# Kernel optimization log

Hardware: AMD Instinct MI355X
Metric: run time of the kernel (lower is better)

Reference implementation:

```python
import jax, jax.numpy as jnp
import numpy as np

D_MODEL = 1024
NUM_HEADS = 16
D_K = D_MODEL // NUM_HEADS
THETA = 10000.0


def _rope(x, pos):
    # x: [B, H, S, D_K], pos: [S]
    angles = 1.0 / (THETA ** (jnp.arange(0, D_K, 2, dtype=jnp.float32) / D_K))  # [D_K/2]
    ang = pos.astype(jnp.float32)[:, None] * angles  # [S, D_K/2]
    cos = jnp.repeat(jnp.cos(ang), 2, axis=-1)  # [S, D_K]
    sin = jnp.repeat(jnp.sin(ang), 2, axis=-1)
    x2 = x.reshape(*x.shape[:-1], D_K // 2, 2)
    xr = jnp.stack([-x2[..., 1], x2[..., 0]], axis=-1).reshape(x.shape)
    return x * cos + xr * sin


def setup_inputs() -> dict:
    key = jax.random.key(0)
    ks = jax.random.split(key, 5)
    B, S = 2, 2048
    sd = np.sqrt(2.0 / (D_MODEL + D_MODEL))
    return {
        "x": jax.random.normal(ks[0], (B, S, D_MODEL), dtype=jnp.float32),
        "token_positions": jnp.arange(S, dtype=jnp.int32),
        "Wq": jax.random.normal(ks[1], (D_MODEL, D_MODEL), dtype=jnp.float32) * sd,
        "Wk": jax.random.normal(ks[2], (D_MODEL, D_MODEL), dtype=jnp.float32) * sd,
        "Wv": jax.random.normal(ks[3], (D_MODEL, D_MODEL), dtype=jnp.float32) * sd,
        "Wo": jax.random.normal(ks[4], (D_MODEL, D_MODEL), dtype=jnp.float32) * sd,
    }


def reference(x, token_positions, Wq, Wk, Wv, Wo):
    B, S, _ = x.shape

    def proj_heads(W):
        y = jnp.einsum('bsd,ed->bse', x, W)  # weight stored [d_out, d_in]
        return y.reshape(B, S, NUM_HEADS, D_K).transpose(0, 2, 1, 3)  # [B,H,S,Dk]

    q = _rope(proj_heads(Wq), token_positions)
    k = _rope(proj_heads(Wk), token_positions)
    v = proj_heads(Wv)

    scores = jnp.einsum('bhqd,bhkd->bhqk', q, k) / np.sqrt(D_K)  # [B,H,S,S]
    causal = jnp.tril(jnp.ones((S, S), dtype=bool))
    scores = jnp.where(causal, scores, -jnp.inf)
    attn = jax.nn.softmax(scores, axis=-1)
    out = jnp.einsum('bhqk,bhkd->bhqd', attn, v)  # [B,H,S,Dk]
    out = out.transpose(0, 2, 1, 3).reshape(B, S, D_MODEL)
    return jnp.einsum('bsd,ed->bse', out, Wo)
```

## Files before the change

kernel.cpp:

```cpp
#include <hip/hip_runtime.h>
#include <hip/hip_bf16.h>
#include <cstdint>
#include <cmath>

#define SEQ 2048
#define NH 16
#define DM 1024
#define BATCH 2

typedef short bf16x8 __attribute__((ext_vector_type(8)));
typedef float f32x4 __attribute__((ext_vector_type(4)));
typedef const void __attribute__((address_space(1)))* gas_t;
typedef void __attribute__((address_space(3)))* las_t;

#if __has_builtin(__builtin_amdgcn_exp2f)
#define EXP2(x) __builtin_amdgcn_exp2f(x)
#else
#define EXP2(x) __expf((x) * 0.6931471805599453f)
#endif

#define QSCALE 0.18033688011112042f

static __device__ __forceinline__ unsigned short f2bf(float f) {
    union { __hip_bfloat16 h; unsigned short u; } cv;
    cv.h = __float2bfloat16(f);
    return cv.u;
}
static __device__ __forceinline__ float bf2f(unsigned short u) {
    union { unsigned short u; __hip_bfloat16 h; } cv;
    cv.u = u;
    return __bfloat162float(cv.h);
}

static __device__ __forceinline__ void gload_lds16(const void* g, void* l) {
    __builtin_amdgcn_global_load_lds(
        reinterpret_cast<gas_t>(reinterpret_cast<uintptr_t>(g)),
        reinterpret_cast<las_t>(reinterpret_cast<uintptr_t>(l)),
        16, 0, 0);
}

__global__ __launch_bounds__(256) void cvt_all(
    const float* __restrict__ x,  const float* __restrict__ wq,
    const float* __restrict__ wk, const float* __restrict__ wv,
    const float* __restrict__ wo,
    unsigned short* __restrict__ xb, unsigned short* __restrict__ wqkv,
    unsigned short* __restrict__ wob) {
    int blk = blockIdx.x;
    const float* src; unsigned short* dst; int base;
    if (blk < 4096)      { src = x;  dst = xb;              base = blk; }
    else if (blk < 5120) { src = wq; dst = wqkv;            base = blk - 4096; }
    else if (blk < 6144) { src = wk; dst = wqkv + 1048576;  base = blk - 5120; }
    else if (blk < 7168) { src = wv; dst = wqkv + 2097152;  base = blk - 6144; }
    else                 { src = wo; dst = wob;             base = blk - 7168; }
    int i = base * 256 + threadIdx.x;
    float4 v = reinterpret_cast<const float4*>(src)[i];
    ushort4 o;
    o.x = f2bf(v.x); o.y = f2bf(v.y); o.z = f2bf(v.z); o.w = f2bf(v.w);
    reinterpret_cast<ushort4*>(dst)[i] = o;
}

template<int OUT_BF16>
__global__ __launch_bounds__(256) void gemm_bt(
    const unsigned short* __restrict__ A,
    const unsigned short* __restrict__ B,
    void* __restrict__ C, int M, int N, int K) {
    __shared__ unsigned short As[128 * 32];
    __shared__ unsigned short Bs[128 * 32];
    const int tid = threadIdx.x;
    const int lane = tid & 63, wid = tid >> 6;
    const int wr = wid >> 1, wc = wid & 1;
    const int ln15 = lane & 15, kq = lane >> 4;
    const int bm = blockIdx.y, bn = blockIdx.x;

    f32x4 acc[4][4] = {};
    const int nk = K >> 5;
    for (int kt = 0; kt < nk; ++kt) {
        #pragma unroll
        for (int i = 0; i < 2; ++i) {
            int c = i * 256 + tid;
            int row = c >> 2, k8 = (c & 3) << 3;
            size_t gofsA = (size_t)(bm * 128 + row) * K + kt * 32 + k8;
            size_t gofsB = (size_t)(bn * 128 + row) * K + kt * 32 + k8;
            unsigned ldsoff = (unsigned)(i * 256 + wid * 64) * 16;
            gload_lds16(A + gofsA, (char*)As + ldsoff);
            gload_lds16(B + gofsB, (char*)Bs + ldsoff);
        }
        __syncthreads();
        bf16x8 af[4], bf[4];
        #pragma unroll
        for (int m = 0; m < 4; ++m)
            af[m] = *reinterpret_cast<const bf16x8*>(&As[(wr * 64 + m * 16 + ln15) * 32 + kq * 8]);
        #pragma unroll
        for (int n = 0; n < 4; ++n)
            bf[n] = *reinterpret_cast<const bf16x8*>(&Bs[(wc * 64 + n * 16 + ln15) * 32 + kq * 8]);
        #pragma unroll
        for (int m = 0; m < 4; ++m)
            #pragma unroll
            for (int n = 0; n < 4; ++n)
                acc[m][n] = __builtin_amdgcn_mfma_f32_16x16x32_bf16(af[m], bf[n], acc[m][n], 0, 0, 0);
        __syncthreads();
    }
    #pragma unroll
    for (int m = 0; m < 4; ++m) {
        #pragma unroll
        for (int n = 0; n < 4; ++n) {
            int col = bn * 128 + wc * 64 + n * 16 + ln15;
            #pragma unroll
            for (int j = 0; j < 4; ++j) {
                int row = bm * 128 + wr * 64 + m * 16 + kq * 4 + j;
                if constexpr (OUT_BF16 != 0)
                    ((unsigned short*)C)[(size_t)row * N + col] = f2bf(acc[m][n][j]);
                else
                    ((float*)C)[(size_t)row * N + col] = acc[m][n][j];
            }
        }
    }
}

__global__ __launch_bounds__(256) void rope_table(const int* __restrict__ pos,
                                                  float2* __restrict__ tab) {
    int idx = blockIdx.x * 256 + threadIdx.x;
    int s = idx >> 5, i = idx & 31;
    float fpos = (float)pos[s];
    float freq = exp2f(-(float)i * (13.287712379549449f / 32.0f));
    float ang = fpos * freq, sn, cs;
    sincosf(ang, &sn, &cs);
    tab[idx] = make_float2(cs, sn);
}

__global__ __launch_bounds__(256) void rope_kernel(
    const unsigned short* __restrict__ qkv, const float2* __restrict__ tab,
    unsigned short* __restrict__ Qh, unsigned short* __restrict__ Kh) {
    int bs = blockIdx.x;
    int b = bs >> 11, s = bs & (SEQ - 1);
    int t = threadIdx.x;
    #pragma unroll
    for (int p = t; p < 512; p += 256) {
        int h = p >> 5, i = p & 31;
        float2 cs = tab[(s << 5) + i];
        size_t src = (size_t)bs * 3072 + h * 64 + 2 * i;
        size_t dst = ((size_t)(b * NH + h) * SEQ + s) * 64 + 2 * i;
        ushort2 qv = *reinterpret_cast<const ushort2*>(qkv + src);
        float q0 = bf2f(qv.x), q1 = bf2f(qv.y);
        ushort2 qo;
        qo.x = f2bf((q0 * cs.x - q1 * cs.y) * QSCALE);
        qo.y = f2bf((q1 * cs.x + q0 * cs.y) * QSCALE);
        *reinterpret_cast<ushort2*>(Qh + dst) = qo;
        ushort2 kv = *reinterpret_cast<const ushort2*>(qkv + src + 1024);
        float k0 = bf2f(kv.x), k1 = bf2f(kv.y);
        ushort2 ko;
        ko.x = f2bf(k0 * cs.x - k1 * cs.y);
        ko.y = f2bf(k1 * cs.x + k0 * cs.y);
        *reinterpret_cast<ushort2*>(Kh + dst) = ko;
    }
}

__global__ __launch_bounds__(256) void vtrans_kernel(
    const unsigned short* __restrict__ qkv, unsigned short* __restrict__ Vo) {
    __shared__ unsigned short tile[64][65];
    int blk = blockIdx.x;
    int st = blk & 31, bh = blk >> 5;
    int sb = st * 64;
    int t = threadIdx.x;
    int b = bh >> 4, h = bh & 15;
    #pragma unroll
    for (int u = t; u < 1024; u += 256) {
        int sl = u >> 4, d4 = (u & 15) << 2;
        ushort4 v = *reinterpret_cast<const ushort4*>(
            qkv + (size_t)(b * SEQ + sb + sl) * 3072 + 2048 + h * 64 + d4);
        tile[sl][d4] = v.x; tile[sl][d4 + 1] = v.y;
        tile[sl][d4 + 2] = v.z; tile[sl][d4 + 3] = v.w;
    }
    __syncthreads();
    #pragma unroll
    for (int u = t; u < 1024; u += 256) {
        int d = u >> 4, s4 = (u & 15) << 2;
        ushort4 o;
        o.x = tile[s4][d]; o.y = tile[s4 + 1][d];
        o.z = tile[s4 + 2][d]; o.w = tile[s4 + 3][d];
        *reinterpret_cast<ushort4*>(Vo + ((size_t)bh * 64 + d) * SEQ + sb + s4) = o;
    }
}

__global__ __launch_bounds__(128) void attn_kernel(
    const unsigned short* __restrict__ Qh, const unsigned short* __restrict__ Kh,
    const unsigned short* __restrict__ Vt, unsigned short* __restrict__ Out) {
    __shared__ unsigned short Kb[2][64 * 64];
    __shared__ unsigned short Vb[2][64 * 64];
    __shared__ unsigned short Plds[2][16 * 72];

    const int tid = threadIdx.x;
    const int wid = tid >> 6, lane = tid & 63;
    const int ln15 = lane & 15, g = lane >> 4;
    const int bid = blockIdx.x;
    const int bh = bid & 31;
    const int pb = bid >> 5;

    const unsigned short* Qp = Qh + (size_t)bh * SEQ * 64;
    const unsigned short* Kp = Kh + (size_t)bh * SEQ * 64;
    const unsigned short* Vp = Vt + (size_t)bh * 64 * SEQ;
    char* Pc = (char*)Plds[wid];

    const unsigned short* kSrc[4];
    const unsigned short* vSrc[4];
    #pragma unroll
    for (int p = 0; p < 4; ++p) {
        int c = tid + (p << 7);
        int row = c >> 3, slot = c & 7;
        kSrc[p] = Kp + (size_t)row * 64 + ((slot ^ (row & 7)) << 3);
        vSrc[p] = Vp + (size_t)row * SEQ + ((slot ^ (row & 7)) << 3);
    }

    auto stage = [&](int kb, int buf) {
        #pragma unroll
        for (int p = 0; p < 4; ++p) {
            unsigned bb = (unsigned)(wid * 1024 + p * 2048);
            gload_lds16(kSrc[p] + (size_t)kb * 64, (char*)Kb[buf] + bb);
            gload_lds16(vSrc[p] + kb, (char*)Vb[buf] + bb);
        }
    };

    unsigned kOff[4][2], vOff[4][2];
    #pragma unroll
    for (int s = 0; s < 4; ++s) {
        int r = ln15 + 16 * s;
        kOff[s][0] = r * 128 + ((g ^ (r & 7)) << 4);
        kOff[s][1] = r * 128 + (((4 + g) ^ (r & 7)) << 4);
    }
    #pragma unroll
    for (int c = 0; c < 4; ++c) {
        int d = c * 16 + ln15;
        vOff[c][0] = d * 128 + ((g ^ (d & 7)) << 4);
        vOff[c][1] = d * 128 + (((4 + g) ^ (d & 7)) << 4);
    }
    const unsigned pW = (unsigned)(ln15 * 144 + 8 * g);
    const unsigned pR = (unsigned)(ln15 * 144 + 16 * g);

    const int b = bh >> 4, h = bh & 15;

    for (int bi = 0; bi < 2; ++bi) {
        const int bnd = bi ? (63 - pb) : pb;
        const int qb = bnd * 32 + wid * 16;
        const int nt = (bnd + 2) >> 1;
        const int thr = qb + ln15 - 4 * g;

        bf16x8 aq0 = *reinterpret_cast<const bf16x8*>(Qp + (size_t)(qb + ln15) * 64 + g * 8);
        bf16x8 aq1 = *reinterpret_cast<const bf16x8*>(Qp + (size_t)(qb + ln15) * 64 + 32 + g * 8);

        f32x4 oacc[4] = {};
        float lsum = 0.f;

        stage(0, 0);

        for (int t = 0; t < nt; ++t) {
            const int kb = t << 6;
            const int cur = t & 1;
            if (t + 1 < nt) {
                stage((t + 1) << 6, cur ^ 1);
                asm volatile("s_waitcnt vmcnt(8)" ::: "memory");
            } else {
                asm volatile("s_waitcnt vmcnt(0)" ::: "memory");
            }
            __builtin_amdgcn_s_barrier();

            const char* K0 = (const char*)Kb[cur];
            const char* V0 = (const char*)Vb[cur];
            bf16x8 kf[8], bv[8];
            #pragma unroll
            for (int s = 0; s < 4; ++s) {
                kf[2 * s]     = *reinterpret_cast<const bf16x8*>(K0 + kOff[s][0]);
                kf[2 * s + 1] = *reinterpret_cast<const bf16x8*>(K0 + kOff[s][1]);
            }
            #pragma unroll
            for (int c = 0; c < 4; ++c) {
                bv[2 * c]     = *reinterpret_cast<const bf16x8*>(V0 + vOff[c][0]);
                bv[2 * c + 1] = *reinterpret_cast<const bf16x8*>(V0 + vOff[c][1]);
            }

            const f32x4 z = {};
            f32x4 sq[4];
            #pragma unroll
            for (int s = 0; s < 4; ++s) {
                sq[s] = __builtin_amdgcn_mfma_f32_16x16x32_bf16(kf[2 * s], aq0, z, 0, 0, 0);
                sq[s] = __builtin_amdgcn_mfma_f32_16x16x32_bf16(kf[2 * s + 1], aq1, sq[s], 0, 0, 0);
            }

            float pv[4][4];
            if (t == nt - 1) {
                #pragma unroll
                for (int s = 0; s < 4; ++s)
                    #pragma unroll
                    for (int j = 0; j < 4; ++j)
                        pv[s][j] = (j <= thr - kb - 16 * s) ? EXP2(sq[s][j]) : 0.f;
            } else {
                #pragma unroll
                for (int s = 0; s < 4; ++s)
                    #pragma unroll
                    for (int j = 0; j < 4; ++j)
                        pv[s][j] = EXP2(sq[s][j]);
            }
            #pragma unroll
            for (int s = 0; s < 4; ++s)
                lsum += (pv[s][0] + pv[s][1]) + (pv[s][2] + pv[s][3]);

            #pragma unroll
            for (int s = 0; s < 4; ++s) {
                ushort4 w;
                w.x = f2bf(pv[s][0]); w.y = f2bf(pv[s][1]);
                w.z = f2bf(pv[s][2]); w.w = f2bf(pv[s][3]);
                *reinterpret_cast<ushort4*>(Pc + pW + 32 * s) = w;
            }
            asm volatile("s_waitcnt lgkmcnt(0)" ::: "memory");
            bf16x8 ap0 = *reinterpret_cast<const bf16x8*>(Pc + pR);
            bf16x8 ap1 = *reinterpret_cast<const bf16x8*>(Pc + pR + 64);
            #pragma unroll
            for (int c = 0; c < 4; ++c) {
                oacc[c] = __builtin_amdgcn_mfma_f32_16x16x32_bf16(ap0, bv[2 * c], oacc[c], 0, 0, 0);
                oacc[c] = __builtin_amdgcn_mfma_f32_16x16x32_bf16(ap1, bv[2 * c + 1], oacc[c], 0, 0, 0);
            }
            asm volatile("s_waitcnt lgkmcnt(0)" ::: "memory");
            __builtin_amdgcn_s_barrier();
        }

        float r = lsum;
        r += __shfl_xor(r, 16);
        r += __shfl_xor(r, 32);
        float linv = 1.f / r;
        float invj[4];
        #pragma unroll
        for (int j = 0; j < 4; ++j)
            invj[j] = __shfl(linv, 20 * g + j);
        #pragma unroll
        for (int c = 0; c < 4; ++c)
            #pragma unroll
            for (int j = 0; j < 4; ++j) {
                int s = qb + g * 4 + j;
                Out[((size_t)(b * SEQ + s)) * DM + h * 64 + c * 16 + ln15] =
                    f2bf(oacc[c][j] * invj[j]);
            }
    }
}

extern "C" void kernel_launch(void* const* d_in, const int* in_sizes, int n_in,
                              void* d_out, int out_size, void* d_ws, size_t ws_size,
                              hipStream_t stream) {
    const float* x = (const float*)d_in[0];
    const int* pos = (const int*)d_in[1];
    const float* Wq = (const float*)d_in[2];
    const float* Wk = (const float*)d_in[3];
    const float* Wv = (const float*)d_in[4];
    const float* Wo = (const float*)d_in[5];
    float* out = (float*)d_out;

    char* ws = (char*)d_ws;
    const size_t MB = 1024 * 1024;
    unsigned short* xb   = (unsigned short*)(ws + 0 * MB);
    unsigned short* wqkv = (unsigned short*)(ws + 8 * MB);
    unsigned short* wob  = (unsigned short*)(ws + 14 * MB);
    unsigned short* qkv  = (unsigned short*)(ws + 16 * MB);
    float2*         tab  = (float2*)       (ws + 40 * MB);
    unsigned short* qh   = (unsigned short*)(ws + 41 * MB);
    unsigned short* kh   = (unsigned short*)(ws + 49 * MB);
    unsigned short* vtr  = (unsigned short*)(ws + 57 * MB);
    unsigned short* att  = (unsigned short*)(ws + 65 * MB);

    cvt_all<<<8192, 256, 0, stream>>>(x, Wq, Wk, Wv, Wo, xb, wqkv, wob);
    rope_table<<<256, 256, 0, stream>>>(pos, tab);

    gemm_bt<1><<<dim3(24, 32), 256, 0, stream>>>(xb, wqkv, qkv, 4096, 3072, 1024);

    rope_kernel<<<4096, 256, 0, stream>>>(qkv, tab, qh, kh);
    vtrans_kernel<<<1024, 256, 0, stream>>>(qkv, vtr);

    attn_kernel<<<1024, 128, 0, stream>>>(qh, kh, vtr, att);

    gemm_bt<0><<<dim3(8, 32), 256, 0, stream>>>(att, wob, out, 4096, 1024, 1024);
}
```

Measured before the change: 128.3 us.

## Use 256x256-tile double-buffered GEMM with 8 waves for QKV projection

Replaces the 128x128-tile GEMM for the fused QKV projection with a new kernel using 256x256 output tiles, 512 threads, swizzled LDS, direct global-to-LDS loads and two-stage double buffering. Larger tiles raise arithmetic intensity and cut redundant global loads of A and B. In exchange, the grid shrinks to 192 blocks, which is fewer than the CU count on MI355X. The kernel also needs 128KB of LDS, which may limit occupancy and leave some CUs idle.

```diff
diff --git a/kernel.cpp b/kernel.cpp
--- a/kernel.cpp
+++ b/kernel.cpp
@@ -117,6 +117,95 @@
     }
 }
 
+__global__ __launch_bounds__(512) void gemm256_bt(
+    const unsigned short* __restrict__ A,
+    const unsigned short* __restrict__ B,
+    unsigned short* __restrict__ C, int M, int N, int K) {
+    __shared__ unsigned short As[2][256 * 64];
+    __shared__ unsigned short Bs[2][256 * 64];
+    const int tid = threadIdx.x;
+    const int lane = tid & 63, wid = tid >> 6;
+    const int wm = wid >> 2, wn = wid & 3;
+    const int ln15 = lane & 15, g = lane >> 4;
+    const int bm = blockIdx.y, bn = blockIdx.x;
+
+    const unsigned short* aSrc[4];
+    const unsigned short* bSrc[4];
+    #pragma unroll
+    for (int p = 0; p < 4; ++p) {
+        int c = tid + (p << 9);
+        int row = c >> 3, slot = c & 7;
+        aSrc[p] = A + (size_t)(bm * 256 + row) * K + ((slot ^ (row & 7)) << 3);
+        bSrc[p] = B + (size_t)(bn * 256 + row) * K + ((slot ^ (row & 7)) << 3);
+    }
+    auto stage = [&](int kt, int buf) {
+        #pragma unroll
+        for (int p = 0; p < 4; ++p) {
+            unsigned dst = (unsigned)(tid + (p << 9)) << 4;
+            gload_lds16(aSrc[p] + kt * 64, (char*)As[buf] + dst);
+            gload_lds16(bSrc[p] + kt * 64, (char*)Bs[buf] + dst);
+        }
+    };
+
+    const unsigned ps0 = (unsigned)((g ^ (ln15 & 7)) << 4);
+    const unsigned ps1 = (unsigned)(((4 + g) ^ (ln15 & 7)) << 4);
+    const unsigned aBase = (unsigned)(wm * 128 + ln15) * 128;
+    const unsigned bBase = (unsigned)(wn * 64 + ln15) * 128;
+
+    f32x4 acc[8][4] = {};
+    const int nkt = K >> 6;
+
+    stage(0, 0);
+    stage(1, 1);
+
+    for (int t = 0; t < nkt; ++t) {
+        const int cur = t & 1;
+        if (t + 1 < nkt) {
+            asm volatile("s_waitcnt vmcnt(8)" ::: "memory");
+        } else {
+            asm volatile("s_waitcnt vmcnt(0)" ::: "memory");
+        }
+        __builtin_amdgcn_s_barrier();
+
+        const char* Ab = (const char*)As[cur];
+        const char* Bb = (const char*)Bs[cur];
+        bf16x8 bf[4][2];
+        #pragma unroll
+        for (int nf = 0; nf < 4; ++nf) {
+            bf[nf][0] = *reinterpret_cast<const bf16x8*>(Bb + bBase + nf * 2048 + ps0);
+            bf[nf][1] = *reinterpret_cast<const bf16x8*>(Bb + bBase + nf * 2048 + ps1);
+        }
+        __builtin_amdgcn_s_setprio(1);
+        #pragma unroll
+        for (int mf = 0; mf < 8; ++mf) {
+            bf16x8 af0 = *reinterpret_cast<const bf16x8*>(Ab + aBase + mf * 2048 + ps0);
+            bf16x8 af1 = *reinterpret_cast<const bf16x8*>(Ab + aBase + mf * 2048 + ps1);
+            #pragma unroll
+            for (int nf = 0; nf < 4; ++nf) {
+                acc[mf][nf] = __builtin_amdgcn_mfma_f32_16x16x32_bf16(af0, bf[nf][0], acc[mf][nf], 0, 0, 0);
+                acc[mf][nf] = __builtin_amdgcn_mfma_f32_16x16x32_bf16(af1, bf[nf][1], acc[mf][nf], 0, 0, 0);
+            }
+        }
+        __builtin_amdgcn_s_setprio(0);
+        asm volatile("s_waitcnt lgkmcnt(0)" ::: "memory");
+        __builtin_amdgcn_s_barrier();
+        if (t + 2 < nkt) stage(t + 2, cur);
+    }
+
+    #pragma unroll
+    for (int mf = 0; mf < 8; ++mf) {
+        #pragma unroll
+        for (int nf = 0; nf < 4; ++nf) {
+            int col = bn * 256 + wn * 64 + nf * 16 + ln15;
+            #pragma unroll
+            for (int j = 0; j < 4; ++j) {
+                int row = bm * 256 + wm * 128 + mf * 16 + g * 4 + j;
+                C[(size_t)row * N + col] = f2bf(acc[mf][nf][j]);
+            }
+        }
+    }
+}
+
 __global__ __launch_bounds__(256) void rope_table(const int* __restrict__ pos,
                                                   float2* __restrict__ tab) {
     int idx = blockIdx.x * 256 + threadIdx.x;
@@ -367,7 +456,7 @@
     cvt_all<<<8192, 256, 0, stream>>>(x, Wq, Wk, Wv, Wo, xb, wqkv, wob);
     rope_table<<<256, 256, 0, stream>>>(pos, tab);
 
-    gemm_bt<1><<<dim3(24, 32), 256, 0, stream>>>(xb, wqkv, qkv, 4096, 3072, 1024);
+    gemm256_bt<<<dim3(12, 16), 512, 0, stream>>>(xb, wqkv, qkv, 4096, 3072, 1024);
 
     rope_kernel<<<4096, 256, 0, stream>>>(qkv, tab, qh, kh);
     vtrans_kernel<<<1024, 256, 0, stream>>>(qkv, vtr);
```

Result: no change. 126.8 us (-1.2%).
